# Performance work log

Hardware: AMD Instinct MI355X
Metric: run time of the kernel (lower is better)

Reference implementation:

```python
import jax, jax.numpy as jnp
import numpy as np

N_NODES = 100000
N_EDGES = 1600000
IN_CH = 64
HID_CH = 64
NUM_LAYERS = 3


def _init_linear(key, out_ch, in_ch, bias=True):
    # torch nn.Linear default init: U(-1/sqrt(in), 1/sqrt(in))
    bound = 1.0 / np.sqrt(in_ch)
    kw, kb = jax.random.split(key)
    W = jax.random.uniform(kw, (out_ch, in_ch), jnp.float32, -bound, bound)
    if bias:
        b = jax.random.uniform(kb, (out_ch,), jnp.float32, -bound, bound)
        return W, b
    return W, None


def setup_inputs() -> dict:
    key = jax.random.key(0)
    ks = jax.random.split(key, 8)
    x = jax.random.normal(ks[0], (N_NODES, IN_CH), jnp.float32)
    edge_index = jax.random.randint(ks[1], (2, N_EDGES), 0, N_NODES, jnp.int64)
    inp = {"x": x, "edge_index": edge_index}
    in_dims = [IN_CH] + [HID_CH] * (NUM_LAYERS - 1)
    for i, d_in in enumerate(in_dims):
        kl, kr = jax.random.split(ks[2 + i])
        Wl, bl = _init_linear(kl, HID_CH, d_in, bias=True)   # lin_l: aggregated neighbors (has bias)
        Wr, _ = _init_linear(kr, HID_CH, d_in, bias=False)   # lin_r: root/self features (no bias)
        inp[f"Wl{i}"] = Wl
        inp[f"bl{i}"] = bl
        inp[f"Wr{i}"] = Wr
    return inp


def _sage_conv(x, src, dst, deg_inv, Wl, bl, Wr):
    # mean aggregation of source features into destination nodes
    msg = x[src]                                              # [E, d]  (irregular gather)
    agg = jax.ops.segment_sum(msg, dst, num_segments=N_NODES)  # [N, d] (irregular scatter)
    agg = agg * deg_inv[:, None]
    return agg @ Wl.T + bl + x @ Wr.T


def reference(x, edge_index, Wl0, bl0, Wr0, Wl1, bl1, Wr1, Wl2, bl2, Wr2):
    src, dst = edge_index[0], edge_index[1]
    deg = jax.ops.segment_sum(jnp.ones((N_EDGES,), x.dtype), dst, num_segments=N_NODES)
    deg_inv = 1.0 / jnp.maximum(deg, 1.0)
    params = [(Wl0, bl0, Wr0), (Wl1, bl1, Wr1), (Wl2, bl2, Wr2)]
    h = x
    for i, (Wl, bl, Wr) in enumerate(params):
        h = _sage_conv(h, src, dst, deg_inv, Wl, bl, Wr)
        if i < NUM_LAYERS - 1:
            h = jax.nn.relu(h)  # dropout is identity in eval mode
    return h
```

## Files before the change

kernel.cpp:

```cpp
#include <hip/hip_runtime.h>
#include <hip/hip_bf16.h>

#define N_NODES 100000
#define N_EDGES 1600000
#define CH 64
#define NPASS 8


__device__ __forceinline__ unsigned short f2bf(float f) {
    unsigned int u = __float_as_uint(f);
    u += 0x7FFF + ((u >> 16) & 1);
    return (unsigned short)(u >> 16);
}
__device__ __forceinline__ float bf2f(unsigned short b) {
    return __uint_as_float(((unsigned int)b) << 16);
}


__global__ void k_hist(const int* __restrict__ dst, int* __restrict__ cnt, int E) {
    int i = blockIdx.x * blockDim.x + threadIdx.x;
    int E4 = E >> 2;
    if (i < E4) {
        int4 d = ((const int4*)dst)[i];
        atomicAdd(&cnt[d.x], 1);
        atomicAdd(&cnt[d.y], 1);
        atomicAdd(&cnt[d.z], 1);
        atomicAdd(&cnt[d.w], 1);
    }
    if (i == 0) for (int e = E4 * 4; e < E; ++e) atomicAdd(&cnt[dst[e]], 1);
}

__global__ __launch_bounds__(1024) void k_scanA(const int* __restrict__ cnt, int N,
                                                int* __restrict__ rowp, int* __restrict__ bsum) {
    __shared__ int s[1024];
    int t = threadIdx.x;
    int g = blockIdx.x * 1024 + t;
    int v = (g < N) ? cnt[g] : 0;
    s[t] = v;
    __syncthreads();
    for (int off = 1; off < 1024; off <<= 1) {
        int x = (t >= off) ? s[t - off] : 0;
        __syncthreads();
        s[t] += x;
        __syncthreads();
    }
    if (g < N) rowp[g] = s[t] - v;
    if (t == 1023) bsum[blockIdx.x] = s[1023];
}

__global__ __launch_bounds__(1024) void k_scanB(int* __restrict__ bsum, int nb) {
    __shared__ int s[1024];
    int t = threadIdx.x;
    int v = (t < nb) ? bsum[t] : 0;
    s[t] = v;
    __syncthreads();
    for (int off = 1; off < 1024; off <<= 1) {
        int x = (t >= off) ? s[t - off] : 0;
        __syncthreads();
        s[t] += x;
        __syncthreads();
    }
    if (t < nb) bsum[t] = s[t] - v;
}

__global__ void k_scanC(int* __restrict__ rowp, const int* __restrict__ cnt,
                        const int* __restrict__ bsum, int* __restrict__ cursor,
                        float* __restrict__ dinv, int N) {
    int g = blockIdx.x * blockDim.x + threadIdx.x;
    if (g < N) {
        int r = rowp[g] + bsum[g >> 10];
        rowp[g]   = r;
        cursor[g] = r;
        int d = cnt[g];
        dinv[g] = 1.0f / (float)(d > 1 ? d : 1);
    }
}

__global__ __launch_bounds__(256) void k_fill(const int* __restrict__ src,
                                              const int* __restrict__ dst,
                                              int* __restrict__ cursor,
                                              int* __restrict__ col, int E, int N) {
    int E4 = E >> 2;
    int tid = blockIdx.x * blockDim.x + threadIdx.x;
    int nth = gridDim.x * blockDim.x;
    int span = (N + NPASS - 1) / NPASS;
    for (int p = 0; p < NPASS; ++p) {
        int lo = p * span, hi = lo + span;
        for (int i = tid; i < E4; i += nth) {
            int4 d = ((const int4*)dst)[i];
            int4 s = ((const int4*)src)[i];
            if (d.x >= lo && d.x < hi) col[atomicAdd(&cursor[d.x], 1)] = s.x;
            if (d.y >= lo && d.y < hi) col[atomicAdd(&cursor[d.y], 1)] = s.y;
            if (d.z >= lo && d.z < hi) col[atomicAdd(&cursor[d.z], 1)] = s.z;
            if (d.w >= lo && d.w < hi) col[atomicAdd(&cursor[d.w], 1)] = s.w;
        }
    }
    if (tid == 0) for (int e = E4 * 4; e < E; ++e)
        col[atomicAdd(&cursor[dst[e]], 1)] = src[e];
}

__global__ __launch_bounds__(256) void k_transform(const float* __restrict__ h,
                                                   const float* __restrict__ Wl,
                                                   const float* __restrict__ bl,
                                                   const float* __restrict__ Wr,
                                                   unsigned short* __restrict__ T,
                                                   float* __restrict__ S, int N) {
    int lane = threadIdx.x & 63;
    float wl[CH], wr[CH];
    const float4* Wl4 = (const float4*)(Wl + lane * CH);
    const float4* Wr4 = (const float4*)(Wr + lane * CH);
#pragma unroll
    for (int q = 0; q < CH / 4; ++q) {
        float4 a = Wl4[q];
        wl[4 * q] = a.x; wl[4 * q + 1] = a.y; wl[4 * q + 2] = a.z; wl[4 * q + 3] = a.w;
        float4 b = Wr4[q];
        wr[4 * q] = b.x; wr[4 * q + 1] = b.y; wr[4 * q + 2] = b.z; wr[4 * q + 3] = b.w;
    }
    float bias = bl[lane];

    int wid    = (blockIdx.x * blockDim.x + threadIdx.x) >> 6;
    int nwaves = (gridDim.x * blockDim.x) >> 6;
    for (int n = wid; n < N; n += nwaves) {
        float hv = h[n * CH + lane];
        float ol = 0.f, orr = 0.f;
#pragma unroll
        for (int c = 0; c < CH; ++c) {
            float hc = __uint_as_float(__builtin_amdgcn_readlane(__float_as_uint(hv), c));
            ol  += hc * wl[c];
            orr += hc * wr[c];
        }
        T[n * CH + lane] = f2bf(ol);
        S[n * CH + lane] = orr + bias;
    }
}

__global__ __launch_bounds__(256) void k_gather(const unsigned short* __restrict__ T,
                                                const float* __restrict__ S,
                                                const int* __restrict__ rowp,
                                                const int* __restrict__ cnt,
                                                const float* __restrict__ dinv,
                                                const int* __restrict__ col,
                                                float* __restrict__ out,
                                                int relu, int N) {
    int wave = threadIdx.x >> 6, lane = threadIdx.x & 63;
    int half = lane >> 5, li = lane & 31;
    int n = blockIdx.x * 4 + wave;
    if (n >= N) return;

    int start = rowp[n];
    int deg   = cnt[n];
    const int* cp = col + start;

    float a0 = 0.f, a1 = 0.f, b0 = 0.f, b1 = 0.f;
    float c0 = 0.f, c1 = 0.f, d0 = 0.f, d1 = 0.f;
    int e = 0;
    for (; e + 8 <= deg; e += 8) {
        int s0 = cp[e + 0 + half];
        int s1 = cp[e + 2 + half];
        int s2 = cp[e + 4 + half];
        int s3 = cp[e + 6 + half];
        unsigned u0 = *(const unsigned*)(T + (size_t)s0 * CH + 2 * li);
        unsigned u1 = *(const unsigned*)(T + (size_t)s1 * CH + 2 * li);
        unsigned u2 = *(const unsigned*)(T + (size_t)s2 * CH + 2 * li);
        unsigned u3 = *(const unsigned*)(T + (size_t)s3 * CH + 2 * li);
        a0 += bf2f((unsigned short)u0); a1 += bf2f((unsigned short)(u0 >> 16));
        b0 += bf2f((unsigned short)u1); b1 += bf2f((unsigned short)(u1 >> 16));
        c0 += bf2f((unsigned short)u2); c1 += bf2f((unsigned short)(u2 >> 16));
        d0 += bf2f((unsigned short)u3); d1 += bf2f((unsigned short)(u3 >> 16));
    }
    for (; e < deg; e += 2) {
        if (e + half < deg) {
            int s = cp[e + half];
            unsigned u = *(const unsigned*)(T + (size_t)s * CH + 2 * li);
            a0 += bf2f((unsigned short)u); a1 += bf2f((unsigned short)(u >> 16));
        }
    }
    float r0 = (a0 + b0) + (c0 + d0);
    float r1 = (a1 + b1) + (c1 + d1);
    r0 += __shfl(r0, lane ^ 32, 64);
    r1 += __shfl(r1, lane ^ 32, 64);

    if (half == 0) {
        float dv = dinv[n];
        float2 sv = *(const float2*)(S + (size_t)n * CH + 2 * li);
        float o0 = sv.x + r0 * dv;
        float o1 = sv.y + r1 * dv;
        if (relu) { o0 = fmaxf(o0, 0.f); o1 = fmaxf(o1, 0.f); }
        *(float2*)(out + (size_t)n * CH + 2 * li) = make_float2(o0, o1);
    }
}


extern "C" void kernel_launch(void* const* d_in, const int* in_sizes, int n_in,
                              void* d_out, int out_size, void* d_ws, size_t ws_size,
                              hipStream_t stream) {
    const float* x   = (const float*)d_in[0];
    const int*   ei  = (const int*)d_in[1];
    const int E = in_sizes[1] / 2;
    const int N = in_sizes[0] / CH;
    const int* src = ei;
    const int* dst = ei + E;

    const float* Wl[3] = { (const float*)d_in[2], (const float*)d_in[5], (const float*)d_in[8] };
    const float* bl[3] = { (const float*)d_in[3], (const float*)d_in[6], (const float*)d_in[9] };
    const float* Wr[3] = { (const float*)d_in[4], (const float*)d_in[7], (const float*)d_in[10] };

    char* ws = (char*)d_ws;
    size_t off = 0;
    auto take = [&](size_t bytes) { char* p = ws + off; off += (bytes + 255) & ~(size_t)255; return p; };
    int*            cnt    = (int*)           take((size_t)N * 4);
    int*            rowp   = (int*)           take((size_t)(N + 1) * 4);
    int*            cursor = (int*)           take((size_t)N * 4);
    float*          dinv   = (float*)         take((size_t)N * 4);
    int*            bsum   = (int*)           take(4096);
    int*            col    = (int*)           take((size_t)E * 4);
    unsigned short* T      = (unsigned short*)take((size_t)N * CH * 2);
    float*          S      = (float*)         take((size_t)N * CH * 4);
    float*          buf0   = (float*)         take((size_t)N * CH * 4);
    float*          outp   = (float*)d_out;

    hipMemsetAsync(cnt, 0, (size_t)N * 4, stream);

    int tb = 256;
    int E4 = E >> 2;
    k_hist<<<(E4 + tb - 1) / tb, tb, 0, stream>>>(dst, cnt, E);

    int nb = (N + 1023) / 1024;
    k_scanA<<<nb, 1024, 0, stream>>>(cnt, N, rowp, bsum);
    k_scanB<<<1, 1024, 0, stream>>>(bsum, nb);
    k_scanC<<<(N + tb - 1) / tb, tb, 0, stream>>>(rowp, cnt, bsum, cursor, dinv, N);

    int fblocks = (E4 + tb - 1) / tb;
    k_fill<<<fblocks, tb, 0, stream>>>(src, dst, cursor, col, E, N);

    int gblocks = (N + 3) / 4;
    k_transform<<<1024, 256, 0, stream>>>(x, Wl[0], bl[0], Wr[0], T, S, N);
    k_gather<<<gblocks, 256, 0, stream>>>(T, S, rowp, cnt, dinv, col, buf0, 1, N);
    k_transform<<<1024, 256, 0, stream>>>(buf0, Wl[1], bl[1], Wr[1], T, S, N);
    k_gather<<<gblocks, 256, 0, stream>>>(T, S, rowp, cnt, dinv, col, buf0, 1, N);
    k_transform<<<1024, 256, 0, stream>>>(buf0, Wl[2], bl[2], Wr[2], T, S, N);
    k_gather<<<gblocks, 256, 0, stream>>>(T, S, rowp, cnt, dinv, col, outp, 0, N);
}
```

Baseline: 581.9 us.

## Partition hist/fill by destination range across blocks; use half-wave per node in gather

The histogram and CSR-fill kernels now run on a fixed grid of 1024 blocks, with each block assigned one of eight destination-node ranges. Edges are filtered by range in parallel, so all ranges are processed concurrently instead of through eight sequential passes, and atomics are localized per range. The gather kernel now maps one node to each 32-lane half-wave, processing 8 nodes per block and walking edges sequentially, which removes the cross-half shuffle reduction. The trade-off is that every block rereads the full edge list and per-node parallelism in the gather is reduced.

```diff
diff --git a/kernel.cpp b/kernel.cpp
--- a/kernel.cpp
+++ b/kernel.cpp
@@ -4,7 +4,7 @@
 #define N_NODES 100000
 #define N_EDGES 1600000
 #define CH 64
-#define NPASS 8
+#define NRANGE 8
 
 
 __device__ __forceinline__ unsigned short f2bf(float f) {
@@ -17,17 +17,23 @@
 }
 
 
-__global__ void k_hist(const int* __restrict__ dst, int* __restrict__ cnt, int E) {
-    int i = blockIdx.x * blockDim.x + threadIdx.x;
+__global__ __launch_bounds__(256) void k_hist(const int* __restrict__ dst,
+                                              int* __restrict__ cnt, int E, int N) {
     int E4 = E >> 2;
-    if (i < E4) {
+    int r    = blockIdx.x & (NRANGE - 1);
+    int gtid = (blockIdx.x >> 3) * blockDim.x + threadIdx.x;
+    int gnth = (gridDim.x >> 3) * blockDim.x;
+    int span = (N + NRANGE - 1) / NRANGE;
+    int lo = r * span, hi = lo + span;
+    for (int i = gtid; i < E4; i += gnth) {
         int4 d = ((const int4*)dst)[i];
-        atomicAdd(&cnt[d.x], 1);
-        atomicAdd(&cnt[d.y], 1);
-        atomicAdd(&cnt[d.z], 1);
-        atomicAdd(&cnt[d.w], 1);
-    }
-    if (i == 0) for (int e = E4 * 4; e < E; ++e) atomicAdd(&cnt[dst[e]], 1);
+        if (d.x >= lo && d.x < hi) atomicAdd(&cnt[d.x], 1);
+        if (d.y >= lo && d.y < hi) atomicAdd(&cnt[d.y], 1);
+        if (d.z >= lo && d.z < hi) atomicAdd(&cnt[d.z], 1);
+        if (d.w >= lo && d.w < hi) atomicAdd(&cnt[d.w], 1);
+    }
+    if (blockIdx.x == 0 && threadIdx.x == 0)
+        for (int e = E4 * 4; e < E; ++e) atomicAdd(&cnt[dst[e]], 1);
 }
 
 __global__ __launch_bounds__(1024) void k_scanA(const int* __restrict__ cnt, int N,
@@ -81,22 +87,22 @@
                                               int* __restrict__ cursor,
                                               int* __restrict__ col, int E, int N) {
     int E4 = E >> 2;
-    int tid = blockIdx.x * blockDim.x + threadIdx.x;
-    int nth = gridDim.x * blockDim.x;
-    int span = (N + NPASS - 1) / NPASS;
-    for (int p = 0; p < NPASS; ++p) {
-        int lo = p * span, hi = lo + span;
-        for (int i = tid; i < E4; i += nth) {
-            int4 d = ((const int4*)dst)[i];
-            int4 s = ((const int4*)src)[i];
-            if (d.x >= lo && d.x < hi) col[atomicAdd(&cursor[d.x], 1)] = s.x;
-            if (d.y >= lo && d.y < hi) col[atomicAdd(&cursor[d.y], 1)] = s.y;
-            if (d.z >= lo && d.z < hi) col[atomicAdd(&cursor[d.z], 1)] = s.z;
-            if (d.w >= lo && d.w < hi) col[atomicAdd(&cursor[d.w], 1)] = s.w;
-        }
-    }
-    if (tid == 0) for (int e = E4 * 4; e < E; ++e)
-        col[atomicAdd(&cursor[dst[e]], 1)] = src[e];
+    int r    = blockIdx.x & (NRANGE - 1);
+    int gtid = (blockIdx.x >> 3) * blockDim.x + threadIdx.x;
+    int gnth = (gridDim.x >> 3) * blockDim.x;
+    int span = (N + NRANGE - 1) / NRANGE;
+    int lo = r * span, hi = lo + span;
+    for (int i = gtid; i < E4; i += gnth) {
+        int4 d = ((const int4*)dst)[i];
+        int4 s = ((const int4*)src)[i];
+        if (d.x >= lo && d.x < hi) col[atomicAdd(&cursor[d.x], 1)] = s.x;
+        if (d.y >= lo && d.y < hi) col[atomicAdd(&cursor[d.y], 1)] = s.y;
+        if (d.z >= lo && d.z < hi) col[atomicAdd(&cursor[d.z], 1)] = s.z;
+        if (d.w >= lo && d.w < hi) col[atomicAdd(&cursor[d.w], 1)] = s.w;
+    }
+    if (blockIdx.x == 0 && threadIdx.x == 0)
+        for (int e = E4 * 4; e < E; ++e)
+            col[atomicAdd(&cursor[dst[e]], 1)] = src[e];
 }
 
 __global__ __launch_bounds__(256) void k_transform(const float* __restrict__ h,
@@ -142,9 +148,8 @@
                                                 const int* __restrict__ col,
                                                 float* __restrict__ out,
                                                 int relu, int N) {
-    int wave = threadIdx.x >> 6, lane = threadIdx.x & 63;
-    int half = lane >> 5, li = lane & 31;
-    int n = blockIdx.x * 4 + wave;
+    int li = threadIdx.x & 31;
+    int n  = blockIdx.x * 8 + (threadIdx.x >> 5);
     if (n >= N) return;
 
     int start = rowp[n];
@@ -154,11 +159,11 @@
     float a0 = 0.f, a1 = 0.f, b0 = 0.f, b1 = 0.f;
     float c0 = 0.f, c1 = 0.f, d0 = 0.f, d1 = 0.f;
     int e = 0;
-    for (; e + 8 <= deg; e += 8) {
-        int s0 = cp[e + 0 + half];
-        int s1 = cp[e + 2 + half];
-        int s2 = cp[e + 4 + half];
-        int s3 = cp[e + 6 + half];
+    for (; e + 4 <= deg; e += 4) {
+        int s0 = cp[e + 0];
+        int s1 = cp[e + 1];
+        int s2 = cp[e + 2];
+        int s3 = cp[e + 3];
         unsigned u0 = *(const unsigned*)(T + (size_t)s0 * CH + 2 * li);
         unsigned u1 = *(const unsigned*)(T + (size_t)s1 * CH + 2 * li);
         unsigned u2 = *(const unsigned*)(T + (size_t)s2 * CH + 2 * li);
@@ -168,26 +173,20 @@
         c0 += bf2f((unsigned short)u2); c1 += bf2f((unsigned short)(u2 >> 16));
         d0 += bf2f((unsigned short)u3); d1 += bf2f((unsigned short)(u3 >> 16));
     }
-    for (; e < deg; e += 2) {
-        if (e + half < deg) {
-            int s = cp[e + half];
-            unsigned u = *(const unsigned*)(T + (size_t)s * CH + 2 * li);
-            a0 += bf2f((unsigned short)u); a1 += bf2f((unsigned short)(u >> 16));
-        }
+    for (; e < deg; ++e) {
+        int s = cp[e];
+        unsigned u = *(const unsigned*)(T + (size_t)s * CH + 2 * li);
+        a0 += bf2f((unsigned short)u); a1 += bf2f((unsigned short)(u >> 16));
     }
     float r0 = (a0 + b0) + (c0 + d0);
     float r1 = (a1 + b1) + (c1 + d1);
-    r0 += __shfl(r0, lane ^ 32, 64);
-    r1 += __shfl(r1, lane ^ 32, 64);
-
-    if (half == 0) {
-        float dv = dinv[n];
-        float2 sv = *(const float2*)(S + (size_t)n * CH + 2 * li);
-        float o0 = sv.x + r0 * dv;
-        float o1 = sv.y + r1 * dv;
-        if (relu) { o0 = fmaxf(o0, 0.f); o1 = fmaxf(o1, 0.f); }
-        *(float2*)(out + (size_t)n * CH + 2 * li) = make_float2(o0, o1);
-    }
+
+    float dv = dinv[n];
+    float2 sv = *(const float2*)(S + (size_t)n * CH + 2 * li);
+    float o0 = sv.x + r0 * dv;
+    float o1 = sv.y + r1 * dv;
+    if (relu) { o0 = fmaxf(o0, 0.f); o1 = fmaxf(o1, 0.f); }
+    *(float2*)(out + (size_t)n * CH + 2 * li) = make_float2(o0, o1);
 }
 
 
@@ -222,18 +221,15 @@
     hipMemsetAsync(cnt, 0, (size_t)N * 4, stream);
 
     int tb = 256;
-    int E4 = E >> 2;
-    k_hist<<<(E4 + tb - 1) / tb, tb, 0, stream>>>(dst, cnt, E);
+    k_hist<<<1024, tb, 0, stream>>>(dst, cnt, E, N);
 
     int nb = (N + 1023) / 1024;
     k_scanA<<<nb, 1024, 0, stream>>>(cnt, N, rowp, bsum);
     k_scanB<<<1, 1024, 0, stream>>>(bsum, nb);
     k_scanC<<<(N + tb - 1) / tb, tb, 0, stream>>>(rowp, cnt, bsum, cursor, dinv, N);
-
-    int fblocks = (E4 + tb - 1) / tb;
-    k_fill<<<fblocks, tb, 0, stream>>>(src, dst, cursor, col, E, N);
-
-    int gblocks = (N + 3) / 4;
+    k_fill<<<1024, tb, 0, stream>>>(src, dst, cursor, col, E, N);
+
+    int gblocks = (N + 7) / 8;
     k_transform<<<1024, 256, 0, stream>>>(x, Wl[0], bl[0], Wr[0], T, S, N);
     k_gather<<<gblocks, 256, 0, stream>>>(T, S, rowp, cnt, dinv, col, buf0, 1, N);
     k_transform<<<1024, 256, 0, stream>>>(buf0, Wl[1], bl[1], Wr[1], T, S, N);
```

After: 535.3 us. -8.0%, faster.
